# Kernel optimization log

Hardware: AMD Instinct MI355X
Metric: run time of the kernel (lower is better)

Reference implementation:

```python
import jax, jax.numpy as jnp
import numpy as np

N_HEADS, D_MODEL, DK, DV = 16, 1024, 64, 64
B, S = 4, 2048
NEG = -1000000000.0


def setup_inputs() -> dict:
    key = jax.random.key(0)
    ks = jax.random.split(key, 10)
    inp = {
        "q": jax.random.normal(ks[0], (B, S, D_MODEL), jnp.float32),
        "k": jax.random.normal(ks[1], (B, S, D_MODEL), jnp.float32),
        "v": jax.random.normal(ks[2], (B, S, D_MODEL), jnp.float32),
        "padding_mask": jax.random.randint(ks[3], (B, 1, S), 0, 2, jnp.int32),
        # linear params (torch Linear: y = x @ W.T + b); store as [in, out]
        "w_q": jax.random.normal(ks[4], (D_MODEL, N_HEADS * DK), jnp.float32) * 0.02,
        "b_q": jnp.zeros((N_HEADS * DK,), jnp.float32),
        "w_k": jax.random.normal(ks[5], (D_MODEL, N_HEADS * DK), jnp.float32) * 0.02,
        "b_k": jnp.zeros((N_HEADS * DK,), jnp.float32),
        "w_v": jax.random.normal(ks[6], (D_MODEL, N_HEADS * DV), jnp.float32) * 0.02,
        "b_v": jnp.zeros((N_HEADS * DV,), jnp.float32),
    }
    return inp


def reference(q, k, v, padding_mask, w_q, b_q, w_k, b_k, w_v, b_v):
    residual = q
    # project and split heads: [B, H, S, dk]
    qh = (q @ w_q + b_q).reshape(B, S, N_HEADS, DK).transpose(0, 2, 1, 3)
    kh = (k @ w_k + b_k).reshape(B, S, N_HEADS, DK).transpose(0, 2, 1, 3)
    vh = (v @ w_v + b_v).reshape(B, S, N_HEADS, DV).transpose(0, 2, 1, 3)
    # NB: original code DIVIDES by factor = dk**-0.5, i.e. multiplies by sqrt(dk)
    scores = jnp.einsum("bhqd,bhkd->bhqk", qh, kh) / (DK ** -0.5)
    mask = padding_mask[:, None, :, :]  # [B,1,1,S] broadcasts over heads/queries
    scores = jnp.where(mask == 0, NEG, scores)
    attn = jax.nn.softmax(scores, axis=-1)  # dropout = identity (eval)
    ctx = jnp.einsum("bhqk,bhkd->bhqd", attn, vh)
    ctx = ctx.transpose(0, 2, 1, 3).reshape(B, S, N_HEADS * DV)
    return ctx + residual
```

## Files before the change

kernel.cpp:

```cpp
#include <hip/hip_runtime.h>
#include <hip/hip_fp16.h>

#define BB 4
#define SS 2048
#define HH 16
#define DKK 64
#define DMODEL 1024

typedef __attribute__((ext_vector_type(8))) _Float16 half8;
typedef __attribute__((ext_vector_type(4))) _Float16 half4;
typedef __attribute__((ext_vector_type(2))) __fp16 fp16x2;
typedef __attribute__((ext_vector_type(4))) float floatx4;

#define MFMA16(a, b, c) __builtin_amdgcn_mfma_f32_16x16x32_f16(a, b, c, 0, 0, 0)

#define SCL2 11.5415603336f

__device__ __forceinline__ void gload_lds16(const _Float16* g, _Float16* l) {
    __builtin_amdgcn_global_load_lds(
        (const __attribute__((address_space(1))) void*)g,
        (__attribute__((address_space(3))) void*)l, 16, 0, 0);
}

__device__ __forceinline__
void convert_x_body(const float* __restrict__ src, _Float16* __restrict__ dst,
                    int bidx)
{
    size_t base = ((size_t)bidx * 256 + threadIdx.x) * 8;
    int m = (int)(base >> 10);
    int kk = (int)(base & 1023);
    float4 a = *(const float4*)(src + base);
    float4 b = *(const float4*)(src + base + 4);
    half8 h;
    h[0] = (_Float16)a.x; h[1] = (_Float16)a.y; h[2] = (_Float16)a.z; h[3] = (_Float16)a.w;
    h[4] = (_Float16)b.x; h[5] = (_Float16)b.y; h[6] = (_Float16)b.z; h[7] = (_Float16)b.w;
    int kd = kk ^ ((m & 7) << 3);
    *(half8*)(dst + ((size_t)m << 10) + kd) = h;
}

__device__ __forceinline__
void convert_wt_body(const float* __restrict__ W, _Float16* __restrict__ WT,
                     int bidx)
{
    __shared__ __attribute__((aligned(16))) _Float16 T[64][72];
    int kt = (bidx >> 4) << 6;
    int nt = (bidx & 15) << 6;
    int tid = threadIdx.x;
    #pragma unroll
    for (int p = 0; p < 4; p++) {
        int lin = tid + p * 256;
        int row = lin >> 4;
        int c4 = (lin & 15) << 2;
        float4 vv = *(const float4*)(W + (size_t)(kt + row) * DMODEL + nt + c4);
        T[c4 + 0][row] = (_Float16)vv.x;
        T[c4 + 1][row] = (_Float16)vv.y;
        T[c4 + 2][row] = (_Float16)vv.z;
        T[c4 + 3][row] = (_Float16)vv.w;
    }
    __syncthreads();
    #pragma unroll
    for (int p = 0; p < 2; p++) {
        int lin = tid + p * 256;
        int nl = lin >> 3;
        int u = lin & 7;
        half8 h = *(const half8*)&T[nl][u * 8];
        int n = nt + nl;
        int kd = kt + ((u ^ (n & 7)) << 3);
        *(half8*)(WT + (size_t)n * DMODEL + kd) = h;
    }
}

__global__ __launch_bounds__(256)
void convert_x(const float* __restrict__ q, const float* __restrict__ k,
               const float* __restrict__ v, _Float16* __restrict__ xq,
               _Float16* __restrict__ xk, _Float16* __restrict__ xv)
{
    int z = blockIdx.y;
    convert_x_body(z == 0 ? q : z == 1 ? k : v,
                   z == 0 ? xq : z == 1 ? xk : xv, blockIdx.x);
}

__global__ __launch_bounds__(256)
void convert_wt(const float* __restrict__ wq, const float* __restrict__ wk,
                const float* __restrict__ wv, _Float16* __restrict__ tq,
                _Float16* __restrict__ tk, _Float16* __restrict__ tv)
{
    int z = blockIdx.y;
    convert_wt_body(z == 0 ? wq : z == 1 ? wk : wv,
                    z == 0 ? tq : z == 1 ? tk : tv, blockIdx.x);
}

__global__ __launch_bounds__(256)
void convert_all(const float* __restrict__ q, const float* __restrict__ k,
                 const float* __restrict__ v, const float* __restrict__ wq,
                 const float* __restrict__ wk, const float* __restrict__ wv,
                 _Float16* __restrict__ xq, _Float16* __restrict__ xk,
                 _Float16* __restrict__ xv, _Float16* __restrict__ tq,
                 _Float16* __restrict__ tk, _Float16* __restrict__ tv)
{
    int y = blockIdx.y;
    if (y < 3) {
        convert_x_body(y == 0 ? q : y == 1 ? k : v,
                       y == 0 ? xq : y == 1 ? xk : xv, blockIdx.x);
    } else {
        if (blockIdx.x >= 768) return;
        int z = blockIdx.x >> 8;
        convert_wt_body(z == 0 ? wq : z == 1 ? wk : wv,
                        z == 0 ? tq : z == 1 ? tk : tv, blockIdx.x & 255);
    }
}

template <int VMODE>
__device__ __forceinline__
void proj_body(const _Float16* __restrict__ X, const _Float16* __restrict__ WT,
               const float* __restrict__ bias, _Float16* __restrict__ out,
               int bidx, float scl)
{
    __shared__ __attribute__((aligned(16))) _Float16 As[128 * 64];
    __shared__ __attribute__((aligned(16))) _Float16 Bs[128 * 64];
    const int tid = threadIdx.x;
    const int wave = tid >> 6, lane = tid & 63, quad = lane >> 4, l16 = lane & 15;
    const int wm = wave >> 1, wn = wave & 1;
    const int m0 = ((bidx & 7) | ((bidx >> 6) << 3)) << 7;
    const int n0 = ((bidx >> 3) & 7) << 7;
    const int lrow = lane >> 3;
    const int lcol = (lane & 7) << 3;

    floatx4 acc[4][4] = {};

    for (int k0 = 0; k0 < DMODEL; k0 += 64) {
        __syncthreads();
        #pragma unroll
        for (int c = 0; c < 4; c++) {
            int row = c * 32 + wave * 8;
            gload_lds16(X + (size_t)(m0 + row + lrow) * DMODEL + k0 + lcol,
                        As + (size_t)row * 64);
            gload_lds16(WT + (size_t)(n0 + row + lrow) * DMODEL + k0 + lcol,
                        Bs + (size_t)row * 64);
        }
        __syncthreads();
        #pragma unroll
        for (int ks = 0; ks < 2; ks++) {
            int ccol = ((ks * 4 + quad) ^ (l16 & 7)) << 3;
            half8 af[4], bf[4];
            #pragma unroll
            for (int i = 0; i < 4; i++)
                af[i] = *(const half8*)(As + (wm * 64 + i * 16 + l16) * 64 + ccol);
            #pragma unroll
            for (int j = 0; j < 4; j++)
                bf[j] = *(const half8*)(Bs + (wn * 64 + j * 16 + l16) * 64 + ccol);
            #pragma unroll
            for (int i = 0; i < 4; i++)
                #pragma unroll
                for (int j = 0; j < 4; j++)
                    acc[i][j] = VMODE ? MFMA16(bf[j], af[i], acc[i][j])
                                      : MFMA16(af[i], bf[j], acc[i][j]);
        }
    }

    if (VMODE == 0) {
        #pragma unroll
        for (int j = 0; j < 4; j++) {
            int ng = n0 + wn * 64 + j * 16 + l16;
            int h = ng >> 6, d = ng & 63;
            float bv = bias[ng];
            #pragma unroll
            for (int i = 0; i < 4; i++)
                #pragma unroll
                for (int r = 0; r < 4; r++) {
                    int mg = m0 + wm * 64 + i * 16 + quad * 4 + r;
                    int bb = mg >> 11, s = mg & 2047;
                    out[(((size_t)bb * HH + h) * SS + s) * DKK + d] =
                        (_Float16)((acc[i][j][r] + bv) * scl);
                }
        }
    } else {
        #pragma unroll
        for (int j = 0; j < 4; j++)
            #pragma unroll
            for (int r = 0; r < 4; r++) {
                int ng = n0 + wn * 64 + j * 16 + quad * 4 + r;
                int h = ng >> 6, d = ng & 63;
                float bv = bias[ng];
                #pragma unroll
                for (int i = 0; i < 4; i++) {
                    int mg = m0 + wm * 64 + i * 16 + l16;
                    int bb = mg >> 11, s = mg & 2047;
                    out[(((size_t)bb * HH + h) * DKK + d) * SS + s] =
                        (_Float16)((acc[i][j][r] + bv) * scl);
                }
            }
    }
}

template <int VMODE>
__global__ __launch_bounds__(256)
void proj128(const _Float16* __restrict__ X, const _Float16* __restrict__ WT,
             const float* __restrict__ bias, _Float16* __restrict__ out, float scl)
{
    proj_body<VMODE>(X, WT, bias, out, blockIdx.x, scl);
}

__global__ __launch_bounds__(256)
void proj_all(const _Float16* __restrict__ Xq, const _Float16* __restrict__ Xk,
              const _Float16* __restrict__ Xv, const _Float16* __restrict__ WTq,
              const _Float16* __restrict__ WTk, const _Float16* __restrict__ WTv,
              const float* __restrict__ bq, const float* __restrict__ bk,
              const float* __restrict__ bv, _Float16* __restrict__ Qh,
              _Float16* __restrict__ Kh, _Float16* __restrict__ VTh)
{
    int z = blockIdx.y;
    if (z == 0)      proj_body<0>(Xq, WTq, bq, Qh, blockIdx.x, SCL2);
    else if (z == 1) proj_body<0>(Xk, WTk, bk, Kh, blockIdx.x, 1.0f);
    else             proj_body<1>(Xv, WTv, bv, VTh, blockIdx.x, 1.0f);
}

__global__ __launch_bounds__(256, 3)
void flash3(const _Float16* __restrict__ Qw, const _Float16* __restrict__ Kw,
            const _Float16* __restrict__ VTw, const int* __restrict__ mask,
            const float* __restrict__ resid, float* __restrict__ out)
{
    __shared__ float Bias[SS];
    __shared__ __attribute__((aligned(16))) _Float16 Plds[4][2][16][64];

    const int tid = threadIdx.x;
    const int wave = tid >> 6, lane = tid & 63, quad = lane >> 4, l16 = lane & 15;
    const int bx = blockIdx.x;
    const int xcd = bx & 7;
    const int jj = bx >> 3;
    const int bh = ((jj >> 4) << 3) | xcd;
    const int qt = jj & 15;
    const int b = bh >> 4;
    const int h = bh & 15;
    const int qbase = qt * 128 + wave * 32;
    const int sw = l16 & 7;

    const int* mk = mask + b * SS;
    for (int i = tid; i < SS; i += 256)
        Bias[i] = mk[i] ? 0.f : -1.0e9f;
    __syncthreads();

    half8 qf[2][2];
    #pragma unroll
    for (int mt = 0; mt < 2; mt++) {
        const _Float16* Qp = Qw + ((size_t)bh * SS + qbase + mt * 16 + l16) * DKK;
        qf[mt][0] = *(const half8*)(Qp + quad * 8);
        qf[mt][1] = *(const half8*)(Qp + 32 + quad * 8);
    }

    float mrow[2] = {-3.0e38f, -3.0e38f};
    float lrow[2] = {0.f, 0.f};
    floatx4 oacc[2][4] = {};

    const _Float16* Kbase = Kw + (size_t)bh * SS * DKK;
    const _Float16* Vbase = VTw + (size_t)bh * DKK * SS;

    for (int kt = 0; kt < SS / 64; kt++) {
        const int kb = kt * 64;

        floatx4 sacc[2][4];
        #pragma unroll
        for (int k2 = 0; k2 < 4; k2++) {
            float4 bv = *(const float4*)&Bias[kb + k2 * 16 + quad * 4];
            floatx4 bi = {bv.x, bv.y, bv.z, bv.w};
            sacc[0][k2] = bi;
            sacc[1][k2] = bi;
        }

        half8 kf[2][4];
        #pragma unroll
        for (int ks = 0; ks < 2; ks++)
            #pragma unroll
            for (int k2 = 0; k2 < 4; k2++)
                kf[ks][k2] = *(const half8*)(Kbase
                    + (size_t)(kb + k2 * 16 + l16) * DKK + ks * 32 + quad * 8);

        #pragma unroll
        for (int mt = 0; mt < 2; mt++)
            #pragma unroll
            for (int ks = 0; ks < 2; ks++)
                #pragma unroll
                for (int k2 = 0; k2 < 4; k2++)
                    sacc[mt][k2] = MFMA16(kf[ks][k2], qf[mt][ks], sacc[mt][k2]);

        half8 vf[2][4];
        #pragma unroll
        for (int ks = 0; ks < 2; ks++)
            #pragma unroll
            for (int dt = 0; dt < 4; dt++)
                vf[ks][dt] = *(const half8*)(Vbase
                    + (size_t)(dt * 16 + l16) * SS + kb + ks * 32 + quad * 8);

        #pragma unroll
        for (int mt = 0; mt < 2; mt++) {
            floatx4* S = sacc[mt];

            float t4[4];
            #pragma unroll
            for (int k2 = 0; k2 < 4; k2++)
                t4[k2] = fmaxf(fmaxf(S[k2][0], S[k2][1]),
                               fmaxf(S[k2][2], S[k2][3]));
            float t = fmaxf(fmaxf(t4[0], t4[1]), fmaxf(t4[2], t4[3]));
            t = fmaxf(t, __shfl_xor(t, 16, 64));
            t = fmaxf(t, __shfl_xor(t, 32, 64));

            if (__ballot(t > mrow[mt])) {
                float mn = fmaxf(mrow[mt], t);
                float al = exp2f(mrow[mt] - mn);
                mrow[mt] = mn;
                lrow[mt] *= al;
                #pragma unroll
                for (int dt = 0; dt < 4; dt++)
                    oacc[mt][dt] *= al;
            }
            const float mn = mrow[mt];

            float ss[4];
            #pragma unroll
            for (int k2 = 0; k2 < 4; k2++) {
                #pragma unroll
                for (int r = 0; r < 4; r++)
                    S[k2][r] = exp2f(S[k2][r] - mn);
                ss[k2] = (S[k2][0] + S[k2][1]) + (S[k2][2] + S[k2][3]);
            }
            float ps = (ss[0] + ss[1]) + (ss[2] + ss[3]);
            ps += __shfl_xor(ps, 16, 64);
            ps += __shfl_xor(ps, 32, 64);
            lrow[mt] += ps;

            #pragma unroll
            for (int k2 = 0; k2 < 4; k2++) {
                union { fp16x2 h2[2]; half4 h4; } u;
                u.h2[0] = __builtin_amdgcn_cvt_pkrtz(S[k2][0], S[k2][1]);
                u.h2[1] = __builtin_amdgcn_cvt_pkrtz(S[k2][2], S[k2][3]);
                int cbw = ((((k2 << 1) | (quad >> 1)) ^ sw) << 3) | ((quad & 1) << 2);
                *(half4*)&Plds[wave][mt][l16][cbw] = u.h4;
            }

            #pragma unroll
            for (int ks = 0; ks < 2; ks++) {
                half8 pf = *(const half8*)
                    &Plds[wave][mt][l16][((ks * 4 + quad) ^ sw) << 3];
                #pragma unroll
                for (int dt = 0; dt < 4; dt++)
                    oacc[mt][dt] = MFMA16(vf[ks][dt], pf, oacc[mt][dt]);
            }
        }
    }

    #pragma unroll
    for (int mt = 0; mt < 2; mt++) {
        float rl = 1.0f / lrow[mt];
        int s = qbase + mt * 16 + l16;
        size_t rowoff = ((size_t)b * SS + s) * DMODEL + h * DKK;
        #pragma unroll
        for (int dt = 0; dt < 4; dt++) {
            size_t gi = rowoff + dt * 16 + quad * 4;
            float4 rv = *(const float4*)&resid[gi];
            float4 ov;
            ov.x = oacc[mt][dt][0] * rl + rv.x;
            ov.y = oacc[mt][dt][1] * rl + rv.y;
            ov.z = oacc[mt][dt][2] * rl + rv.z;
            ov.w = oacc[mt][dt][3] * rl + rv.w;
            *(float4*)&out[gi] = ov;
        }
    }
}

extern "C" void kernel_launch(void* const* d_in, const int* in_sizes, int n_in,
                              void* d_out, int out_size, void* d_ws, size_t ws_size,
                              hipStream_t stream)
{
    const float* q    = (const float*)d_in[0];
    const float* k    = (const float*)d_in[1];
    const float* v    = (const float*)d_in[2];
    const int*   mask = (const int*)d_in[3];
    const float* wq   = (const float*)d_in[4];
    const float* bq   = (const float*)d_in[5];
    const float* wk   = (const float*)d_in[6];
    const float* bk   = (const float*)d_in[7];
    const float* wv   = (const float*)d_in[8];
    const float* bv   = (const float*)d_in[9];
    float* out = (float*)d_out;

    const size_t TENS = (size_t)BB * SS * HH * DKK;
    const size_t WSZ  = (size_t)DMODEL * DMODEL;
    _Float16* base = (_Float16*)d_ws;

    bool big = ws_size >= (6 * TENS + 3 * WSZ) * sizeof(_Float16);
    _Float16 *Xq, *Xk, *Xv, *Qh, *Kh, *VTh, *WTq;
    if (big) {
        Xq = base;            Xk = base + TENS;     Xv = base + 2 * TENS;
        Qh = base + 3 * TENS; Kh = base + 4 * TENS; VTh = base + 5 * TENS;
        WTq = base + 6 * TENS;
    } else {
        Xq = base;            Xk = base + TENS;     Xv = base + 2 * TENS;
        Qh = base + 3 * TENS; Kh = Xq;              VTh = Xk;
        WTq = base + 4 * TENS;
    }
    _Float16* WTk = WTq + WSZ;
    _Float16* WTv = WTk + WSZ;

    if (big) {
        hipLaunchKernelGGL(convert_all, dim3(4096, 4), dim3(256), 0, stream,
                           q, k, v, wq, wk, wv, Xq, Xk, Xv, WTq, WTk, WTv);
        hipLaunchKernelGGL(proj_all, dim3(512, 3), dim3(256), 0, stream,
                           Xq, Xk, Xv, WTq, WTk, WTv, bq, bk, bv, Qh, Kh, VTh);
    } else {
        hipLaunchKernelGGL(convert_x, dim3(4096, 3), dim3(256), 0, stream,
                           q, k, v, Xq, Xk, Xv);
        hipLaunchKernelGGL(convert_wt, dim3(256, 3), dim3(256), 0, stream,
                           wq, wk, wv, WTq, WTk, WTv);
        hipLaunchKernelGGL((proj128<0>), dim3(512), dim3(256), 0, stream, Xq, WTq, bq, Qh, SCL2);
        hipLaunchKernelGGL((proj128<0>), dim3(512), dim3(256), 0, stream, Xk, WTk, bk, Kh, 1.0f);
        hipLaunchKernelGGL((proj128<1>), dim3(512), dim3(256), 0, stream, Xv, WTv, bv, VTh, 1.0f);
    }
    hipLaunchKernelGGL(flash3, dim3(BB * HH * (SS / 128)), dim3(256), 0, stream,
                       Qh, Kh, VTh, mask, q, out);
}
```

Measured before the change: 510.1 us.

## Double-buffer K/V tiles in LDS via async global loads with swizzled layout

The attention kernel now stages each 64-key K and V^T tile into double-buffered LDS with global_load_lds, prefetching the next tile while the current one is computed. The projection kernels write K and V^T with an XOR swizzle so the LDS reads are bank-conflict free. Previously every wave read K and V straight from global memory. The online-softmax rescale is now unconditional instead of guarded by a ballot, and the P stores are interleaved with the exp computation. The extra 32KB of LDS and the removed occupancy hint of 3 blocks may reduce occupancy, and two barriers are added per iteration.

```diff
diff --git a/kernel.cpp b/kernel.cpp
--- a/kernel.cpp
+++ b/kernel.cpp
@@ -110,7 +110,7 @@
     }
 }
 
-template <int VMODE>
+template <int VMODE, int SWZ>
 __device__ __forceinline__
 void proj_body(const _Float16* __restrict__ X, const _Float16* __restrict__ WT,
                const float* __restrict__ bias, _Float16* __restrict__ out,
@@ -170,7 +170,8 @@
                 for (int r = 0; r < 4; r++) {
                     int mg = m0 + wm * 64 + i * 16 + quad * 4 + r;
                     int bb = mg >> 11, s = mg & 2047;
-                    out[(((size_t)bb * HH + h) * SS + s) * DKK + d] =
+                    int dd = SWZ ? ((((d >> 3) ^ (s & 7)) << 3) | (d & 7)) : d;
+                    out[(((size_t)bb * HH + h) * SS + s) * DKK + dd] =
                         (_Float16)((acc[i][j][r] + bv) * scl);
                 }
         }
@@ -186,19 +187,20 @@
                 for (int i = 0; i < 4; i++) {
                     int mg = m0 + wm * 64 + i * 16 + l16;
                     int bb = mg >> 11, s = mg & 2047;
-                    out[(((size_t)bb * HH + h) * DKK + d) * SS + s] =
+                    int ss2 = SWZ ? (s ^ ((d & 7) << 3)) : s;
+                    out[(((size_t)bb * HH + h) * DKK + d) * SS + ss2] =
                         (_Float16)((acc[i][j][r] + bv) * scl);
                 }
             }
     }
 }
 
-template <int VMODE>
+template <int VMODE, int SWZ>
 __global__ __launch_bounds__(256)
 void proj128(const _Float16* __restrict__ X, const _Float16* __restrict__ WT,
              const float* __restrict__ bias, _Float16* __restrict__ out, float scl)
 {
-    proj_body<VMODE>(X, WT, bias, out, blockIdx.x, scl);
+    proj_body<VMODE, SWZ>(X, WT, bias, out, blockIdx.x, scl);
 }
 
 __global__ __launch_bounds__(256)
@@ -210,18 +212,20 @@
               _Float16* __restrict__ Kh, _Float16* __restrict__ VTh)
 {
     int z = blockIdx.y;
-    if (z == 0)      proj_body<0>(Xq, WTq, bq, Qh, blockIdx.x, SCL2);
-    else if (z == 1) proj_body<0>(Xk, WTk, bk, Kh, blockIdx.x, 1.0f);
-    else             proj_body<1>(Xv, WTv, bv, VTh, blockIdx.x, 1.0f);
-}
-
-__global__ __launch_bounds__(256, 3)
+    if (z == 0)      proj_body<0, 0>(Xq, WTq, bq, Qh, blockIdx.x, SCL2);
+    else if (z == 1) proj_body<0, 1>(Xk, WTk, bk, Kh, blockIdx.x, 1.0f);
+    else             proj_body<1, 1>(Xv, WTv, bv, VTh, blockIdx.x, 1.0f);
+}
+
+__global__ __launch_bounds__(256)
 void flash3(const _Float16* __restrict__ Qw, const _Float16* __restrict__ Kw,
             const _Float16* __restrict__ VTw, const int* __restrict__ mask,
             const float* __restrict__ resid, float* __restrict__ out)
 {
     __shared__ float Bias[SS];
     __shared__ __attribute__((aligned(16))) _Float16 Plds[4][2][16][64];
+    __shared__ __attribute__((aligned(16))) _Float16 Ks[2][4096];
+    __shared__ __attribute__((aligned(16))) _Float16 Vs[2][4096];
 
     const int tid = threadIdx.x;
     const int wave = tid >> 6, lane = tid & 63, quad = lane >> 4, l16 = lane & 15;
@@ -235,10 +239,8 @@
     const int qbase = qt * 128 + wave * 32;
     const int sw = l16 & 7;
 
-    const int* mk = mask + b * SS;
-    for (int i = tid; i < SS; i += 256)
-        Bias[i] = mk[i] ? 0.f : -1.0e9f;
-    __syncthreads();
+    const _Float16* Kbase = Kw + (size_t)bh * SS * DKK;
+    const _Float16* Vbase = VTw + (size_t)bh * DKK * SS;
 
     half8 qf[2][2];
     #pragma unroll
@@ -248,15 +250,46 @@
         qf[mt][1] = *(const half8*)(Qp + 32 + quad * 8);
     }
 
+    #pragma unroll
+    for (int c = 0; c < 2; c++) {
+        int chunk = wave * 2 + c;
+        gload_lds16(Kbase + chunk * 512 + lane * 8, &Ks[0][chunk * 512]);
+        gload_lds16(Vbase + (size_t)(chunk * 8 + (lane >> 3)) * SS + (lane & 7) * 8,
+                    &Vs[0][chunk * 512]);
+    }
+
+    const int* mk = mask + b * SS;
+    for (int i = tid; i < SS; i += 256)
+        Bias[i] = mk[i] ? 0.f : -1.0e9f;
+    asm volatile("s_waitcnt lgkmcnt(0)" ::: "memory");
+    __builtin_amdgcn_s_barrier();
+
     float mrow[2] = {-3.0e38f, -3.0e38f};
     float lrow[2] = {0.f, 0.f};
     floatx4 oacc[2][4] = {};
 
-    const _Float16* Kbase = Kw + (size_t)bh * SS * DKK;
-    const _Float16* Vbase = VTw + (size_t)bh * DKK * SS;
-
     for (int kt = 0; kt < SS / 64; kt++) {
-        const int kb = kt * 64;
+        const int cur = kt & 1;
+        const _Float16* Kl = Ks[cur];
+        const _Float16* Vl = Vs[cur];
+        const int kb = kt << 6;
+
+        if (kt < SS / 64 - 1) {
+            const int kb1 = kb + 64;
+            #pragma unroll
+            for (int c = 0; c < 2; c++) {
+                int chunk = wave * 2 + c;
+                gload_lds16(Kbase + (size_t)kb1 * DKK + chunk * 512 + lane * 8,
+                            &Ks[cur ^ 1][chunk * 512]);
+                gload_lds16(Vbase + (size_t)(chunk * 8 + (lane >> 3)) * SS + kb1
+                                + (lane & 7) * 8,
+                            &Vs[cur ^ 1][chunk * 512]);
+            }
+            asm volatile("s_waitcnt vmcnt(4)" ::: "memory");
+        } else {
+            asm volatile("s_waitcnt vmcnt(0)" ::: "memory");
+        }
+        __builtin_amdgcn_s_barrier();
 
         floatx4 sacc[2][4];
         #pragma unroll
@@ -272,8 +305,8 @@
         for (int ks = 0; ks < 2; ks++)
             #pragma unroll
             for (int k2 = 0; k2 < 4; k2++)
-                kf[ks][k2] = *(const half8*)(Kbase
-                    + (size_t)(kb + k2 * 16 + l16) * DKK + ks * 32 + quad * 8);
+                kf[ks][k2] = *(const half8*)(Kl + (k2 * 16 + l16) * 64
+                                + (((ks * 4 + quad) ^ sw) << 3));
 
         #pragma unroll
         for (int mt = 0; mt < 2; mt++)
@@ -288,8 +321,8 @@
         for (int ks = 0; ks < 2; ks++)
             #pragma unroll
             for (int dt = 0; dt < 4; dt++)
-                vf[ks][dt] = *(const half8*)(Vbase
-                    + (size_t)(dt * 16 + l16) * SS + kb + ks * 32 + quad * 8);
+                vf[ks][dt] = *(const half8*)(Vl + (dt * 16 + l16) * 64
+                                + (((ks * 4 + quad) ^ sw) << 3));
 
         #pragma unroll
         for (int mt = 0; mt < 2; mt++) {
@@ -304,16 +337,9 @@
             t = fmaxf(t, __shfl_xor(t, 16, 64));
             t = fmaxf(t, __shfl_xor(t, 32, 64));
 
-            if (__ballot(t > mrow[mt])) {
-                float mn = fmaxf(mrow[mt], t);
-                float al = exp2f(mrow[mt] - mn);
-                mrow[mt] = mn;
-                lrow[mt] *= al;
-                #pragma unroll
-                for (int dt = 0; dt < 4; dt++)
-                    oacc[mt][dt] *= al;
-            }
-            const float mn = mrow[mt];
+            float mn = fmaxf(mrow[mt], t);
+            float al = exp2f(mrow[mt] - mn);
+            mrow[mt] = mn;
 
             float ss[4];
             #pragma unroll
@@ -321,21 +347,21 @@
                 #pragma unroll
                 for (int r = 0; r < 4; r++)
                     S[k2][r] = exp2f(S[k2][r] - mn);
+                union { fp16x2 h2[2]; half4 h4; } u;
+                u.h2[0] = __builtin_amdgcn_cvt_pkrtz(S[k2][0], S[k2][1]);
+                u.h2[1] = __builtin_amdgcn_cvt_pkrtz(S[k2][2], S[k2][3]);
+                int cbw = ((((k2 << 1) | (quad >> 1)) ^ sw) << 3) | ((quad & 1) << 2);
+                *(half4*)&Plds[wave][mt][l16][cbw] = u.h4;
                 ss[k2] = (S[k2][0] + S[k2][1]) + (S[k2][2] + S[k2][3]);
             }
             float ps = (ss[0] + ss[1]) + (ss[2] + ss[3]);
             ps += __shfl_xor(ps, 16, 64);
             ps += __shfl_xor(ps, 32, 64);
-            lrow[mt] += ps;
-
-            #pragma unroll
-            for (int k2 = 0; k2 < 4; k2++) {
-                union { fp16x2 h2[2]; half4 h4; } u;
-                u.h2[0] = __builtin_amdgcn_cvt_pkrtz(S[k2][0], S[k2][1]);
-                u.h2[1] = __builtin_amdgcn_cvt_pkrtz(S[k2][2], S[k2][3]);
-                int cbw = ((((k2 << 1) | (quad >> 1)) ^ sw) << 3) | ((quad & 1) << 2);
-                *(half4*)&Plds[wave][mt][l16][cbw] = u.h4;
-            }
+            lrow[mt] = lrow[mt] * al + ps;
+
+            #pragma unroll
+            for (int dt = 0; dt < 4; dt++)
+                oacc[mt][dt] *= al;
 
             #pragma unroll
             for (int ks = 0; ks < 2; ks++) {
@@ -346,6 +372,7 @@
                     oacc[mt][dt] = MFMA16(vf[ks][dt], pf, oacc[mt][dt]);
             }
         }
+        __builtin_amdgcn_s_barrier();
     }
 
     #pragma unroll
@@ -411,9 +438,9 @@
                            q, k, v, Xq, Xk, Xv);
         hipLaunchKernelGGL(convert_wt, dim3(256, 3), dim3(256), 0, stream,
                            wq, wk, wv, WTq, WTk, WTv);
-        hipLaunchKernelGGL((proj128<0>), dim3(512), dim3(256), 0, stream, Xq, WTq, bq, Qh, SCL2);
-        hipLaunchKernelGGL((proj128<0>), dim3(512), dim3(256), 0, stream, Xk, WTk, bk, Kh, 1.0f);
-        hipLaunchKernelGGL((proj128<1>), dim3(512), dim3(256), 0, stream, Xv, WTv, bv, VTh, 1.0f);
+        hipLaunchKernelGGL((proj128<0, 0>), dim3(512), dim3(256), 0, stream, Xq, WTq, bq, Qh, SCL2);
+        hipLaunchKernelGGL((proj128<0, 1>), dim3(512), dim3(256), 0, stream, Xk, WTk, bk, Kh, 1.0f);
+        hipLaunchKernelGGL((proj128<1, 1>), dim3(512), dim3(256), 0, stream, Xv, WTv, bv, VTh, 1.0f);
     }
     hipLaunchKernelGGL(flash3, dim3(BB * HH * (SS / 128)), dim3(256), 0, stream,
                        Qh, Kh, VTh, mask, q, out);
```

New measurement: 515.8 us. No clear change (+1.1%).
